# Optimization experiments

Hardware: AMD Instinct MI355X
Metric: run time of the kernel (lower is better)

Reference implementation:

```python
import jax, jax.numpy as jnp
import numpy as np
import math

D_MODEL = 512
N_TOTAL = 1024
HW = 4096
EPSILON = 0.2
NUM_HEADS = 8
D_K = D_MODEL // NUM_HEADS
BATCH = 4


def setup_inputs() -> dict:
    rng = jax.random.key(0)
    ks = jax.random.split(rng, 16)
    s = 1.0 / math.sqrt(D_MODEL)
    inp = {
        "query": jax.random.normal(ks[0], (BATCH, N_TOTAL, D_MODEL), jnp.float32),
        "key": jax.random.normal(ks[1], (BATCH, HW, D_MODEL), jnp.float32),
        "value": jax.random.normal(ks[2], (BATCH, HW, D_MODEL), jnp.float32),
        "x_tilde": jax.random.uniform(ks[3], (HW, 2), jnp.float32),
        "x_hat": jax.random.uniform(ks[4], (N_TOTAL, HW, 2), jnp.float32),
        # torch nn.Linear params: W is (out, in), y = x @ W.T + b
        "Wq": jax.random.uniform(ks[5], (D_MODEL, D_MODEL), jnp.float32, -s, s),
        "bq": jax.random.uniform(ks[6], (D_MODEL,), jnp.float32, -s, s),
        "Wk": jax.random.uniform(ks[7], (D_MODEL, D_MODEL), jnp.float32, -s, s),
        "bk": jax.random.uniform(ks[8], (D_MODEL,), jnp.float32, -s, s),
        "Wv": jax.random.uniform(ks[9], (D_MODEL, D_MODEL), jnp.float32, -s, s),
        "bv": jax.random.uniform(ks[10], (D_MODEL,), jnp.float32, -s, s),
        "Wo": jax.random.uniform(ks[11], (D_MODEL, D_MODEL), jnp.float32, -s, s),
        "bo": jax.random.uniform(ks[12], (D_MODEL,), jnp.float32, -s, s),
    }
    return inp


def _geo_mask(x_tilde, x_hat):
    # x_tilde: (HW, 2), x_hat: (N_total, HW, 2)
    diff = x_tilde[None, :, :] - x_hat            # (N, HW, 2)
    dist = jnp.sqrt(jnp.sum(diff * diff, axis=-1))  # (N, HW)
    return jnp.where(dist < EPSILON, 0.0, -jnp.inf).astype(x_hat.dtype)


def reference(query, key, value, x_tilde, x_hat, Wq, bq, Wk, bk, Wv, bv, Wo, bo):
    B = query.shape[0]
    M_geo = _geo_mask(x_tilde, x_hat)  # (N, HW)

    def heads(x, W, b):
        y = x @ W.T + b                                   # (B, L, D)
        return y.reshape(B, -1, NUM_HEADS, D_K).transpose(0, 2, 1, 3)  # (B, H, L, dk)

    Q = heads(query, Wq, bq)   # (B, H, N, dk)
    K = heads(key, Wk, bk)     # (B, H, HW, dk)
    V = heads(value, Wv, bv)   # (B, H, HW, dk)

    scores = jnp.einsum("bhnd,bhmd->bhnm", Q, K) / math.sqrt(D_K)
    scores = scores + M_geo[None, None, :, :]
    attn = jax.nn.softmax(scores, axis=-1)                # (B, H, N, HW)
    ctx = jnp.einsum("bhnm,bhmd->bhnd", attn, V)          # (B, H, N, dk)
    ctx = ctx.transpose(0, 2, 1, 3).reshape(B, -1, D_MODEL)
    out = ctx @ Wo.T + bo                                 # (B, N, D)
    return out, attn
```

## Files before the change

kernel.cpp:

```cpp
#include <hip/hip_runtime.h>
#include <cstdint>
#include <cstddef>

typedef __attribute__((ext_vector_type(4))) float f32x4;
typedef __attribute__((ext_vector_type(8))) short s16x8;
typedef __attribute__((ext_vector_type(4))) short s16x4;
typedef unsigned short u16;
typedef unsigned long long u64;

static __device__ inline u16 f2bf(float f) {
    unsigned u = __builtin_bit_cast(unsigned, f);
    u += 0x7fffu + ((u >> 16) & 1u);
    return (u16)(u >> 16);
}

static __device__ inline f32x4 mfma16(s16x8 a, s16x8 b, f32x4 c) {
    return __builtin_amdgcn_mfma_f32_16x16x32_bf16(a, b, c, 0, 0, 0);
}

static __device__ inline float redsum16(float v) {
    v += __shfl_xor(v, 1);
    v += __shfl_xor(v, 2);
    v += __shfl_xor(v, 4);
    v += __shfl_xor(v, 8);
    return v;
}

__global__ __launch_bounds__(256) void cvt_bf16_kernel(const float* __restrict__ src,
                                                       u16* __restrict__ dst, float scale) {
    int i = (blockIdx.x * 256 + threadIdx.x) * 4;
    f32x4 v = *(const f32x4*)(src + i);
    s16x4 o;
    o[0] = (short)f2bf(v[0] * scale); o[1] = (short)f2bf(v[1] * scale);
    o[2] = (short)f2bf(v[2] * scale); o[3] = (short)f2bf(v[3] * scale);
    *(s16x4*)(dst + i) = o;
}

__global__ __launch_bounds__(256) void mask_kernel(const float* __restrict__ xt,
                                                   const float* __restrict__ xh,
                                                   u64* __restrict__ mb) {
    int tid  = threadIdx.x;
    int lane = tid & 63;
    int wv   = blockIdx.x * 4 + (tid >> 6);
    int n    = wv >> 6;
    int mbk  = wv & 63;
    int m    = (mbk << 6) + lane;
    size_t hidx = ((size_t)n * 4096 + m) * 2;
    float dx = xt[2 * m]     - xh[hidx];
    float dy = xt[2 * m + 1] - xh[hidx + 1];
    bool p = sqrtf(dx * dx + dy * dy) < 0.2f;
    u64 bal = __ballot(p);
    if (lane == 0) mb[wv] = bal;
}

template <int INF32, int MODE, int LSHIFT>
__global__ __launch_bounds__(256) void proj_kernel(const void* __restrict__ Xv,
                                                   const u16* __restrict__ Wb,
                                                   const float* __restrict__ bias,
                                                   float bscale,
                                                   void* __restrict__ Yv) {
    __shared__ u16 aT[128 * 72];
    __shared__ u16 bT[128 * 72];

    int tid  = threadIdx.x;
    int lane = tid & 63, w = tid >> 6, q = lane >> 4, m15 = lane & 15;
    int wm = w >> 1, wn = w & 1;
    int m0 = blockIdx.x * 128, n0 = blockIdx.y * 128;
    int sRow = tid >> 1, sC = (tid & 1) * 32;

    f32x4 acc[4][4];
#pragma unroll
    for (int i = 0; i < 4; ++i)
#pragma unroll
        for (int j = 0; j < 4; ++j) { f32x4 z = {0.f, 0.f, 0.f, 0.f}; acc[i][j] = z; }

    for (int kb = 0; kb < 512; kb += 64) {
        if (INF32) {
            const float* X = (const float*)Xv;
#pragma unroll
            for (int j = 0; j < 8; ++j) {
                int col = sC + j * 4;
                f32x4 v = *(const f32x4*)(X + (size_t)(m0 + sRow) * 512 + kb + col);
                s16x4 o;
                o[0] = (short)f2bf(v[0]); o[1] = (short)f2bf(v[1]);
                o[2] = (short)f2bf(v[2]); o[3] = (short)f2bf(v[3]);
                *(s16x4*)(aT + sRow * 72 + col) = o;
            }
        } else {
            const u16* X = (const u16*)Xv;
#pragma unroll
            for (int j = 0; j < 4; ++j) {
                int col = sC + j * 8;
                s16x8 v = *(const s16x8*)(X + (size_t)(m0 + sRow) * 512 + kb + col);
                *(s16x8*)(aT + sRow * 72 + col) = v;
            }
        }
#pragma unroll
        for (int j = 0; j < 4; ++j) {
            int col = sC + j * 8;
            s16x8 v = *(const s16x8*)(Wb + (size_t)(n0 + sRow) * 512 + kb + col);
            *(s16x8*)(bT + sRow * 72 + col) = v;
        }
        __syncthreads();
#pragma unroll
        for (int kk = 0; kk < 2; ++kk) {
            s16x8 af[4], bf[4];
#pragma unroll
            for (int t = 0; t < 4; ++t) {
                af[t] = *(const s16x8*)(aT + (wm * 64 + t * 16 + m15) * 72 + kk * 32 + q * 8);
                bf[t] = *(const s16x8*)(bT + (wn * 64 + t * 16 + m15) * 72 + kk * 32 + q * 8);
            }
#pragma unroll
            for (int am = 0; am < 4; ++am)
#pragma unroll
                for (int bn = 0; bn < 4; ++bn)
                    acc[am][bn] = mfma16(af[am], bf[bn], acc[am][bn]);
        }
        __syncthreads();
    }

#pragma unroll
    for (int am = 0; am < 4; ++am) {
        int mg = m0 + wm * 64 + am * 16 + q * 4;
#pragma unroll
        for (int bn = 0; bn < 4; ++bn) {
            int col = n0 + wn * 64 + bn * 16 + m15;
            float bv = bias[col] * bscale;
            if (MODE == 2) {
                float* Y = (float*)Yv;
#pragma unroll
                for (int r = 0; r < 4; ++r)
                    Y[(size_t)(mg + r) * 512 + col] = acc[am][bn][r] + bv;
            } else if (MODE == 3) {
                u16* Y = (u16*)Yv;
                int hh = col >> 6, d = col & 63;
#pragma unroll
                for (int r = 0; r < 4; ++r) {
                    int m = mg + r;
                    int bb = m >> LSHIFT;
                    int nn = m & ((1 << LSHIFT) - 1);
                    Y[(((size_t)(bb * 8 + hh) << LSHIFT) + nn) * 64 + d] = f2bf(acc[am][bn][r] + bv);
                }
            } else {
                u16* Yt = (u16*)Yv;
                int bidx = mg >> 12, hw0 = mg & 4095;
                int hh = col >> 6, d = col & 63;
                s16x4 o;
#pragma unroll
                for (int r = 0; r < 4; ++r) o[r] = (short)f2bf(acc[am][bn][r] + bv);
                *(s16x4*)(Yt + ((size_t)((bidx << 3) + hh) * 64 + d) * 4096 + hw0) = o;
            }
        }
    }
}

__global__ __launch_bounds__(512) void attn_kernel(const u16* __restrict__ Qh,
                                                   const u16* __restrict__ Kh,
                                                   const u16* __restrict__ Vt,
                                                   const u64* __restrict__ mbits,
                                                   float* __restrict__ attnO,
                                                   u16* __restrict__ ctxO) {
    __shared__ u64   smask[2048];
    __shared__ float sred[8][32];
    __shared__ float srowi[32];
    __shared__ u16   sps[8][2][16 * 72];
    __shared__ float sctx[2048];

    int tid  = threadIdx.x;
    int lane = tid & 63, w = tid >> 6, q = lane >> 4, m15 = lane & 15;
    int i = blockIdx.x;
    int jj = i >> 3;
    int bh = (i & 7) * 4 + (jj & 3);
    int n0 = (jj >> 2) * 32;
    int b = bh >> 3, h = bh & 7;

    for (int t = tid; t < 2048; t += 512) {
        smask[t] = mbits[(size_t)n0 * 64 + t];
        sctx[t]  = 0.f;
    }
    __syncthreads();

    s16x8 aQ[2][2];
#pragma unroll
    for (int g = 0; g < 2; ++g) {
        const u16* Qp = Qh + (((size_t)bh << 10) + n0 + g * 16 + m15) * 64 + q * 8;
        aQ[g][0] = *(const s16x8*)(Qp);
        aQ[g][1] = *(const s16x8*)(Qp + 32);
    }

    const u16* Kp = Kh + (((size_t)bh << 12) + (w << 9) + m15) * 64 + q * 8;
    const float L2E = 1.44269504f;

    float ls[2][4] = {{0.f,0.f,0.f,0.f},{0.f,0.f,0.f,0.f}};
    for (int t4 = 0; t4 < 8; ++t4) {
        int widx = w * 8 + t4;
        u64 mk[2][4];
#pragma unroll
        for (int g = 0; g < 2; ++g)
#pragma unroll
            for (int r = 0; r < 4; ++r) mk[g][r] = smask[(g * 16 + q * 4 + r) * 64 + widx];
#pragma unroll
        for (int tt = 0; tt < 4; ++tt) {
            const u16* kp = Kp + (size_t)(t4 * 4 + tt) * (16 * 64);
            s16x8 b0 = *(const s16x8*)(kp);
            s16x8 b1 = *(const s16x8*)(kp + 32);
            f32x4 z = {0.f, 0.f, 0.f, 0.f};
            f32x4 c0 = mfma16(aQ[0][0], b0, mfma16(aQ[0][1], b1, z));
            f32x4 c1 = mfma16(aQ[1][0], b0, mfma16(aQ[1][1], b1, z));
            int bit = tt * 16 + m15;
#pragma unroll
            for (int r = 0; r < 4; ++r) {
                float p0 = ((mk[0][r] >> bit) & 1ull) ? exp2f(c0[r] * L2E) : 0.f;
                float p1 = ((mk[1][r] >> bit) & 1ull) ? exp2f(c1[r] * L2E) : 0.f;
                ls[0][r] += p0;
                ls[1][r] += p1;
            }
        }
    }
#pragma unroll
    for (int g = 0; g < 2; ++g)
#pragma unroll
        for (int r = 0; r < 4; ++r) {
            float v = redsum16(ls[g][r]);
            if (m15 == 0) sred[w][g * 16 + q * 4 + r] = v;
        }
    __syncthreads();
    if (tid < 32) {
        float ss = 0.f;
#pragma unroll
        for (int ww = 0; ww < 8; ++ww) ss += sred[ww][tid];
        srowi[tid] = 1.0f / ss;
    }
    __syncthreads();
    float iv[2][4];
#pragma unroll
    for (int g = 0; g < 2; ++g)
#pragma unroll
        for (int r = 0; r < 4; ++r) iv[g][r] = srowi[g * 16 + q * 4 + r];

    const u16* Vp = Vt + (((size_t)bh << 6) + m15) * 4096 + (w << 9) + q * 8;
    float* aBp[2];
#pragma unroll
    for (int g = 0; g < 2; ++g)
        aBp[g] = attnO + (((size_t)bh << 10) + n0 + g * 16 + q * 4) * 4096 + (w << 9) + m15;

    f32x4 ctxa[2][4];
#pragma unroll
    for (int g = 0; g < 2; ++g)
#pragma unroll
        for (int dt = 0; dt < 4; ++dt) { f32x4 z = {0.f, 0.f, 0.f, 0.f}; ctxa[g][dt] = z; }

    for (int cc = 0; cc < 8; ++cc) {
        int widx = w * 8 + cc;
        u64 mk[2][4];
#pragma unroll
        for (int g = 0; g < 2; ++g)
#pragma unroll
            for (int r = 0; r < 4; ++r) mk[g][r] = smask[(g * 16 + q * 4 + r) * 64 + widx];

        f32x4 cs[2][4];
#pragma unroll
        for (int tt = 0; tt < 4; ++tt) {
            const u16* kp = Kp + (size_t)(cc * 4 + tt) * (16 * 64);
            s16x8 b0 = *(const s16x8*)(kp);
            s16x8 b1 = *(const s16x8*)(kp + 32);
            f32x4 z = {0.f, 0.f, 0.f, 0.f};
            f32x4 c0 = mfma16(aQ[0][0], b0, mfma16(aQ[0][1], b1, z));
            f32x4 c1 = mfma16(aQ[1][0], b0, mfma16(aQ[1][1], b1, z));
            int bit = tt * 16 + m15;
#pragma unroll
            for (int r = 0; r < 4; ++r) {
                float p0 = ((mk[0][r] >> bit) & 1ull) ? exp2f(c0[r] * L2E) : 0.f;
                float p1 = ((mk[1][r] >> bit) & 1ull) ? exp2f(c1[r] * L2E) : 0.f;
                sps[w][0][(q * 4 + r) * 72 + tt * 16 + m15] = f2bf(p0);
                sps[w][1][(q * 4 + r) * 72 + tt * 16 + m15] = f2bf(p1);
                cs[0][tt][r] = p0 * iv[0][r];
                cs[1][tt][r] = p1 * iv[1][r];
            }
        }
#pragma unroll
        for (int g = 0; g < 2; ++g)
#pragma unroll
            for (int half = 0; half < 2; ++half) {
                s16x8 aP = *(const s16x8*)(&sps[w][g][m15 * 72 + half * 32 + q * 8]);
#pragma unroll
                for (int dt = 0; dt < 4; ++dt) {
                    s16x8 bV = *(const s16x8*)(Vp + (size_t)dt * (16 * 4096) + cc * 64 + half * 32);
                    ctxa[g][dt] = mfma16(aP, bV, ctxa[g][dt]);
                }
            }
#pragma unroll
        for (int g = 0; g < 2; ++g)
#pragma unroll
            for (int tt = 0; tt < 4; ++tt)
#pragma unroll
                for (int r = 0; r < 4; ++r)
                    aBp[g][(size_t)r * 4096 + cc * 64 + tt * 16] = cs[g][tt][r];
    }

#pragma unroll
    for (int g = 0; g < 2; ++g)
#pragma unroll
        for (int dt = 0; dt < 4; ++dt)
#pragma unroll
            for (int r = 0; r < 4; ++r)
                atomicAdd(&sctx[(g * 16 + q * 4 + r) * 64 + dt * 16 + m15],
                          ctxa[g][dt][r] * iv[g][r]);
    __syncthreads();
    for (int t = tid; t < 2048; t += 512) {
        int rr = t >> 6, d = t & 63;
        ctxO[(((size_t)b << 10) + n0 + rr) * 512 + h * 64 + d] = f2bf(sctx[t]);
    }
}

extern "C" void kernel_launch(void* const* d_in, const int* in_sizes, int n_in,
                              void* d_out, int out_size, void* d_ws, size_t ws_size,
                              hipStream_t stream) {
    (void)in_sizes; (void)n_in; (void)out_size; (void)ws_size;
    const float* query = (const float*)d_in[0];
    const float* key   = (const float*)d_in[1];
    const float* value = (const float*)d_in[2];
    const float* x_tilde = (const float*)d_in[3];
    const float* x_hat   = (const float*)d_in[4];
    const float* Wq = (const float*)d_in[5];  const float* bq = (const float*)d_in[6];
    const float* Wk = (const float*)d_in[7];  const float* bk = (const float*)d_in[8];
    const float* Wv = (const float*)d_in[9];  const float* bv = (const float*)d_in[10];
    const float* Wo = (const float*)d_in[11]; const float* bo = (const float*)d_in[12];

    char* ws = (char*)d_ws;
    u16* wq   = (u16*)(ws + 0);
    u16* wk   = (u16*)(ws + 524288);
    u16* wv   = (u16*)(ws + 1048576);
    u16* wo   = (u16*)(ws + 1572864);
    u16* Qh   = (u16*)(ws + 2097152);
    u16* Kh   = (u16*)(ws + 6291456);
    u16* Vtb  = (u16*)(ws + 23068672);
    u16* ctxb = (u16*)(ws + 39845888);
    u64* mbits = (u64*)(ws + 44040192);

    cvt_bf16_kernel<<<256, 256, 0, stream>>>(Wq, wq, 0.125f);
    cvt_bf16_kernel<<<256, 256, 0, stream>>>(Wk, wk, 1.0f);
    cvt_bf16_kernel<<<256, 256, 0, stream>>>(Wv, wv, 1.0f);
    cvt_bf16_kernel<<<256, 256, 0, stream>>>(Wo, wo, 1.0f);
    mask_kernel<<<16384, 256, 0, stream>>>(x_tilde, x_hat, mbits);

    proj_kernel<1, 3, 10><<<dim3(32, 4),  256, 0, stream>>>(query, wq, bq, 0.125f, Qh);
    proj_kernel<1, 3, 12><<<dim3(128, 4), 256, 0, stream>>>(key,   wk, bk, 1.0f,   Kh);
    proj_kernel<1, 1, 12><<<dim3(128, 4), 256, 0, stream>>>(value, wv, bv, 1.0f,   Vtb);

    float* attnO = (float*)d_out + 2097152;
    attn_kernel<<<1024, 512, 0, stream>>>(Qh, Kh, Vtb, mbits, attnO, ctxb);

    proj_kernel<0, 2, 10><<<dim3(32, 4), 256, 0, stream>>>(ctxb, wo, bo, 1.0f, d_out);
}
```

Before: 924.3 us.

## Cache unnormalized fp16 probabilities in registers instead of recomputing QK in attention

Attention now caches the packed fp16 exponentials from the first pass in registers, so the second pass no longer recomputes QK^T and exp. The whole pipeline moves from bf16 to fp16 MFMA. The block tile is halved to 16 query rows with twice as many blocks, and the large attention-matrix writes use nontemporal stores. In exchange there is higher register pressure (64 unsigneds per thread) and fp16 range limits on the exponentials, since scores are not max-subtracted and could overflow fp16.

```diff
diff --git a/kernel.cpp b/kernel.cpp
--- a/kernel.cpp
+++ b/kernel.cpp
@@ -3,19 +3,20 @@
 #include <cstddef>
 
 typedef __attribute__((ext_vector_type(4))) float f32x4;
+typedef __attribute__((ext_vector_type(8))) _Float16 h16x8;
+typedef __attribute__((ext_vector_type(2))) _Float16 h16x2;
 typedef __attribute__((ext_vector_type(8))) short s16x8;
 typedef __attribute__((ext_vector_type(4))) short s16x4;
 typedef unsigned short u16;
 typedef unsigned long long u64;
 
-static __device__ inline u16 f2bf(float f) {
-    unsigned u = __builtin_bit_cast(unsigned, f);
-    u += 0x7fffu + ((u >> 16) & 1u);
-    return (u16)(u >> 16);
-}
-
-static __device__ inline f32x4 mfma16(s16x8 a, s16x8 b, f32x4 c) {
-    return __builtin_amdgcn_mfma_f32_16x16x32_bf16(a, b, c, 0, 0, 0);
+static __device__ inline u16 f2h(float f) {
+    _Float16 h = (_Float16)f;
+    return __builtin_bit_cast(u16, h);
+}
+
+static __device__ inline f32x4 mfma16(h16x8 a, h16x8 b, f32x4 c) {
+    return __builtin_amdgcn_mfma_f32_16x16x32_f16(a, b, c, 0, 0, 0);
 }
 
 static __device__ inline float redsum16(float v) {
@@ -26,13 +27,13 @@
     return v;
 }
 
-__global__ __launch_bounds__(256) void cvt_bf16_kernel(const float* __restrict__ src,
-                                                       u16* __restrict__ dst, float scale) {
+__global__ __launch_bounds__(256) void cvt_h_kernel(const float* __restrict__ src,
+                                                    u16* __restrict__ dst, float scale) {
     int i = (blockIdx.x * 256 + threadIdx.x) * 4;
     f32x4 v = *(const f32x4*)(src + i);
     s16x4 o;
-    o[0] = (short)f2bf(v[0] * scale); o[1] = (short)f2bf(v[1] * scale);
-    o[2] = (short)f2bf(v[2] * scale); o[3] = (short)f2bf(v[3] * scale);
+    o[0] = (short)f2h(v[0] * scale); o[1] = (short)f2h(v[1] * scale);
+    o[2] = (short)f2h(v[2] * scale); o[3] = (short)f2h(v[3] * scale);
     *(s16x4*)(dst + i) = o;
 }
 
@@ -82,8 +83,8 @@
                 int col = sC + j * 4;
                 f32x4 v = *(const f32x4*)(X + (size_t)(m0 + sRow) * 512 + kb + col);
                 s16x4 o;
-                o[0] = (short)f2bf(v[0]); o[1] = (short)f2bf(v[1]);
-                o[2] = (short)f2bf(v[2]); o[3] = (short)f2bf(v[3]);
+                o[0] = (short)f2h(v[0]); o[1] = (short)f2h(v[1]);
+                o[2] = (short)f2h(v[2]); o[3] = (short)f2h(v[3]);
                 *(s16x4*)(aT + sRow * 72 + col) = o;
             }
         } else {
@@ -104,11 +105,11 @@
         __syncthreads();
 #pragma unroll
         for (int kk = 0; kk < 2; ++kk) {
-            s16x8 af[4], bf[4];
+            h16x8 af[4], bf[4];
 #pragma unroll
             for (int t = 0; t < 4; ++t) {
-                af[t] = *(const s16x8*)(aT + (wm * 64 + t * 16 + m15) * 72 + kk * 32 + q * 8);
-                bf[t] = *(const s16x8*)(bT + (wn * 64 + t * 16 + m15) * 72 + kk * 32 + q * 8);
+                af[t] = *(const h16x8*)(aT + (wm * 64 + t * 16 + m15) * 72 + kk * 32 + q * 8);
+                bf[t] = *(const h16x8*)(bT + (wn * 64 + t * 16 + m15) * 72 + kk * 32 + q * 8);
             }
 #pragma unroll
             for (int am = 0; am < 4; ++am)
@@ -139,7 +140,7 @@
                     int m = mg + r;
                     int bb = m >> LSHIFT;
                     int nn = m & ((1 << LSHIFT) - 1);
-                    Y[(((size_t)(bb * 8 + hh) << LSHIFT) + nn) * 64 + d] = f2bf(acc[am][bn][r] + bv);
+                    Y[(((size_t)(bb * 8 + hh) << LSHIFT) + nn) * 64 + d] = f2h(acc[am][bn][r] + bv);
                 }
             } else {
                 u16* Yt = (u16*)Yv;
@@ -147,7 +148,7 @@
                 int hh = col >> 6, d = col & 63;
                 s16x4 o;
 #pragma unroll
-                for (int r = 0; r < 4; ++r) o[r] = (short)f2bf(acc[am][bn][r] + bv);
+                for (int r = 0; r < 4; ++r) o[r] = (short)f2h(acc[am][bn][r] + bv);
                 *(s16x4*)(Yt + ((size_t)((bidx << 3) + hh) * 64 + d) * 4096 + hw0) = o;
             }
         }
@@ -160,156 +161,122 @@
                                                    const u64* __restrict__ mbits,
                                                    float* __restrict__ attnO,
                                                    u16* __restrict__ ctxO) {
-    __shared__ u64   smask[2048];
-    __shared__ float sred[8][32];
-    __shared__ float srowi[32];
-    __shared__ u16   sps[8][2][16 * 72];
-    __shared__ float sctx[2048];
+    __shared__ u64   smask[1024];
+    __shared__ float sred[8][16];
+    __shared__ float srowi[16];
+    __shared__ u16   sps[8][16 * 72];
+    __shared__ float sctx[1024];
 
     int tid  = threadIdx.x;
     int lane = tid & 63, w = tid >> 6, q = lane >> 4, m15 = lane & 15;
     int i = blockIdx.x;
     int jj = i >> 3;
     int bh = (i & 7) * 4 + (jj & 3);
-    int n0 = (jj >> 2) * 32;
+    int n0 = (jj >> 2) * 16;
     int b = bh >> 3, h = bh & 7;
 
-    for (int t = tid; t < 2048; t += 512) {
+    for (int t = tid; t < 1024; t += 512) {
         smask[t] = mbits[(size_t)n0 * 64 + t];
         sctx[t]  = 0.f;
     }
     __syncthreads();
 
-    s16x8 aQ[2][2];
-#pragma unroll
-    for (int g = 0; g < 2; ++g) {
-        const u16* Qp = Qh + (((size_t)bh << 10) + n0 + g * 16 + m15) * 64 + q * 8;
-        aQ[g][0] = *(const s16x8*)(Qp);
-        aQ[g][1] = *(const s16x8*)(Qp + 32);
+    h16x8 aQ[2];
+    {
+        const u16* Qp = Qh + (((size_t)bh << 10) + n0 + m15) * 64 + q * 8;
+        aQ[0] = *(const h16x8*)(Qp);
+        aQ[1] = *(const h16x8*)(Qp + 32);
     }
 
     const u16* Kp = Kh + (((size_t)bh << 12) + (w << 9) + m15) * 64 + q * 8;
     const float L2E = 1.44269504f;
 
-    float ls[2][4] = {{0.f,0.f,0.f,0.f},{0.f,0.f,0.f,0.f}};
-    for (int t4 = 0; t4 < 8; ++t4) {
-        int widx = w * 8 + t4;
-        u64 mk[2][4];
-#pragma unroll
-        for (int g = 0; g < 2; ++g)
-#pragma unroll
-            for (int r = 0; r < 4; ++r) mk[g][r] = smask[(g * 16 + q * 4 + r) * 64 + widx];
+    unsigned st[8][8];
+    float ls[4] = {0.f, 0.f, 0.f, 0.f};
+#pragma unroll
+    for (int cc = 0; cc < 8; ++cc) {
+        int widx = w * 8 + cc;
+        u64 mk[4];
+#pragma unroll
+        for (int r = 0; r < 4; ++r) mk[r] = smask[(q * 4 + r) * 64 + widx];
 #pragma unroll
         for (int tt = 0; tt < 4; ++tt) {
-            const u16* kp = Kp + (size_t)(t4 * 4 + tt) * (16 * 64);
-            s16x8 b0 = *(const s16x8*)(kp);
-            s16x8 b1 = *(const s16x8*)(kp + 32);
+            const u16* kp = Kp + (size_t)(cc * 4 + tt) * (16 * 64);
+            h16x8 b0 = *(const h16x8*)(kp);
+            h16x8 b1 = *(const h16x8*)(kp + 32);
             f32x4 z = {0.f, 0.f, 0.f, 0.f};
-            f32x4 c0 = mfma16(aQ[0][0], b0, mfma16(aQ[0][1], b1, z));
-            f32x4 c1 = mfma16(aQ[1][0], b0, mfma16(aQ[1][1], b1, z));
+            f32x4 c0 = mfma16(aQ[0], b0, mfma16(aQ[1], b1, z));
             int bit = tt * 16 + m15;
+            float p[4];
 #pragma unroll
             for (int r = 0; r < 4; ++r) {
-                float p0 = ((mk[0][r] >> bit) & 1ull) ? exp2f(c0[r] * L2E) : 0.f;
-                float p1 = ((mk[1][r] >> bit) & 1ull) ? exp2f(c1[r] * L2E) : 0.f;
-                ls[0][r] += p0;
-                ls[1][r] += p1;
-            }
-        }
-    }
-#pragma unroll
-    for (int g = 0; g < 2; ++g)
-#pragma unroll
-        for (int r = 0; r < 4; ++r) {
-            float v = redsum16(ls[g][r]);
-            if (m15 == 0) sred[w][g * 16 + q * 4 + r] = v;
-        }
+                p[r] = ((mk[r] >> bit) & 1ull) ? exp2f(c0[r] * L2E) : 0.f;
+                ls[r] += p[r];
+            }
+            st[cc][tt * 2 + 0] = __builtin_bit_cast(unsigned, __builtin_amdgcn_cvt_pkrtz(p[0], p[1]));
+            st[cc][tt * 2 + 1] = __builtin_bit_cast(unsigned, __builtin_amdgcn_cvt_pkrtz(p[2], p[3]));
+        }
+    }
+#pragma unroll
+    for (int r = 0; r < 4; ++r) {
+        float v = redsum16(ls[r]);
+        if (m15 == 0) sred[w][q * 4 + r] = v;
+    }
     __syncthreads();
-    if (tid < 32) {
+    if (tid < 16) {
         float ss = 0.f;
 #pragma unroll
         for (int ww = 0; ww < 8; ++ww) ss += sred[ww][tid];
         srowi[tid] = 1.0f / ss;
     }
     __syncthreads();
-    float iv[2][4];
-#pragma unroll
-    for (int g = 0; g < 2; ++g)
-#pragma unroll
-        for (int r = 0; r < 4; ++r) iv[g][r] = srowi[g * 16 + q * 4 + r];
+    float iv[4];
+#pragma unroll
+    for (int r = 0; r < 4; ++r) iv[r] = srowi[q * 4 + r];
 
     const u16* Vp = Vt + (((size_t)bh << 6) + m15) * 4096 + (w << 9) + q * 8;
-    float* aBp[2];
-#pragma unroll
-    for (int g = 0; g < 2; ++g)
-        aBp[g] = attnO + (((size_t)bh << 10) + n0 + g * 16 + q * 4) * 4096 + (w << 9) + m15;
-
-    f32x4 ctxa[2][4];
-#pragma unroll
-    for (int g = 0; g < 2; ++g)
-#pragma unroll
-        for (int dt = 0; dt < 4; ++dt) { f32x4 z = {0.f, 0.f, 0.f, 0.f}; ctxa[g][dt] = z; }
-
+    float* aBp = attnO + (((size_t)bh << 10) + n0 + q * 4) * 4096 + (w << 9) + m15;
+
+    f32x4 ctxa[4];
+#pragma unroll
+    for (int dt = 0; dt < 4; ++dt) { f32x4 z = {0.f, 0.f, 0.f, 0.f}; ctxa[dt] = z; }
+
+#pragma unroll
     for (int cc = 0; cc < 8; ++cc) {
-        int widx = w * 8 + cc;
-        u64 mk[2][4];
-#pragma unroll
-        for (int g = 0; g < 2; ++g)
-#pragma unroll
-            for (int r = 0; r < 4; ++r) mk[g][r] = smask[(g * 16 + q * 4 + r) * 64 + widx];
-
-        f32x4 cs[2][4];
 #pragma unroll
         for (int tt = 0; tt < 4; ++tt) {
-            const u16* kp = Kp + (size_t)(cc * 4 + tt) * (16 * 64);
-            s16x8 b0 = *(const s16x8*)(kp);
-            s16x8 b1 = *(const s16x8*)(kp + 32);
-            f32x4 z = {0.f, 0.f, 0.f, 0.f};
-            f32x4 c0 = mfma16(aQ[0][0], b0, mfma16(aQ[0][1], b1, z));
-            f32x4 c1 = mfma16(aQ[1][0], b0, mfma16(aQ[1][1], b1, z));
-            int bit = tt * 16 + m15;
-#pragma unroll
-            for (int r = 0; r < 4; ++r) {
-                float p0 = ((mk[0][r] >> bit) & 1ull) ? exp2f(c0[r] * L2E) : 0.f;
-                float p1 = ((mk[1][r] >> bit) & 1ull) ? exp2f(c1[r] * L2E) : 0.f;
-                sps[w][0][(q * 4 + r) * 72 + tt * 16 + m15] = f2bf(p0);
-                sps[w][1][(q * 4 + r) * 72 + tt * 16 + m15] = f2bf(p1);
-                cs[0][tt][r] = p0 * iv[0][r];
-                cs[1][tt][r] = p1 * iv[1][r];
-            }
-        }
-#pragma unroll
-        for (int g = 0; g < 2; ++g)
-#pragma unroll
-            for (int half = 0; half < 2; ++half) {
-                s16x8 aP = *(const s16x8*)(&sps[w][g][m15 * 72 + half * 32 + q * 8]);
-#pragma unroll
-                for (int dt = 0; dt < 4; ++dt) {
-                    s16x8 bV = *(const s16x8*)(Vp + (size_t)dt * (16 * 4096) + cc * 64 + half * 32);
-                    ctxa[g][dt] = mfma16(aP, bV, ctxa[g][dt]);
-                }
-            }
-#pragma unroll
-        for (int g = 0; g < 2; ++g)
-#pragma unroll
-            for (int tt = 0; tt < 4; ++tt)
-#pragma unroll
-                for (int r = 0; r < 4; ++r)
-                    aBp[g][(size_t)r * 4096 + cc * 64 + tt * 16] = cs[g][tt][r];
-    }
-
-#pragma unroll
-    for (int g = 0; g < 2; ++g)
-#pragma unroll
-        for (int dt = 0; dt < 4; ++dt)
-#pragma unroll
-            for (int r = 0; r < 4; ++r)
-                atomicAdd(&sctx[(g * 16 + q * 4 + r) * 64 + dt * 16 + m15],
-                          ctxa[g][dt][r] * iv[g][r]);
+#pragma unroll
+            for (int j = 0; j < 2; ++j) {
+                unsigned u = st[cc][tt * 2 + j];
+                sps[w][(q * 4 + j * 2 + 0) * 72 + tt * 16 + m15] = (u16)(u & 0xffffu);
+                sps[w][(q * 4 + j * 2 + 1) * 72 + tt * 16 + m15] = (u16)(u >> 16);
+                h16x2 hv = __builtin_bit_cast(h16x2, u);
+                float f0 = (float)hv[0] * iv[j * 2 + 0];
+                float f1 = (float)hv[1] * iv[j * 2 + 1];
+                __builtin_nontemporal_store(f0, aBp + (size_t)(j * 2 + 0) * 4096 + cc * 64 + tt * 16);
+                __builtin_nontemporal_store(f1, aBp + (size_t)(j * 2 + 1) * 4096 + cc * 64 + tt * 16);
+            }
+        }
+#pragma unroll
+        for (int half = 0; half < 2; ++half) {
+            h16x8 aP = *(const h16x8*)(&sps[w][m15 * 72 + half * 32 + q * 8]);
+#pragma unroll
+            for (int dt = 0; dt < 4; ++dt) {
+                h16x8 bV = *(const h16x8*)(Vp + (size_t)dt * (16 * 4096) + cc * 64 + half * 32);
+                ctxa[dt] = mfma16(aP, bV, ctxa[dt]);
+            }
+        }
+    }
+
+#pragma unroll
+    for (int dt = 0; dt < 4; ++dt)
+#pragma unroll
+        for (int r = 0; r < 4; ++r)
+            atomicAdd(&sctx[(q * 4 + r) * 64 + dt * 16 + m15], ctxa[dt][r] * iv[r]);
     __syncthreads();
-    for (int t = tid; t < 2048; t += 512) {
+    for (int t = tid; t < 1024; t += 512) {
         int rr = t >> 6, d = t & 63;
-        ctxO[(((size_t)b << 10) + n0 + rr) * 512 + h * 64 + d] = f2bf(sctx[t]);
+        ctxO[(((size_t)b << 10) + n0 + rr) * 512 + h * 64 + d] = f2h(sctx[t]);
     }
 }
 
@@ -338,10 +305,10 @@
     u16* ctxb = (u16*)(ws + 39845888);
     u64* mbits = (u64*)(ws + 44040192);
 
-    cvt_bf16_kernel<<<256, 256, 0, stream>>>(Wq, wq, 0.125f);
-    cvt_bf16_kernel<<<256, 256, 0, stream>>>(Wk, wk, 1.0f);
-    cvt_bf16_kernel<<<256, 256, 0, stream>>>(Wv, wv, 1.0f);
-    cvt_bf16_kernel<<<256, 256, 0, stream>>>(Wo, wo, 1.0f);
+    cvt_h_kernel<<<256, 256, 0, stream>>>(Wq, wq, 0.125f);
+    cvt_h_kernel<<<256, 256, 0, stream>>>(Wk, wk, 1.0f);
+    cvt_h_kernel<<<256, 256, 0, stream>>>(Wv, wv, 1.0f);
+    cvt_h_kernel<<<256, 256, 0, stream>>>(Wo, wo, 1.0f);
     mask_kernel<<<16384, 256, 0, stream>>>(x_tilde, x_hat, mbits);
 
     proj_kernel<1, 3, 10><<<dim3(32, 4),  256, 0, stream>>>(query, wq, bq, 0.125f, Qh);
@@ -349,7 +316,7 @@
     proj_kernel<1, 1, 12><<<dim3(128, 4), 256, 0, stream>>>(value, wv, bv, 1.0f,   Vtb);
 
     float* attnO = (float*)d_out + 2097152;
-    attn_kernel<<<1024, 512, 0, stream>>>(Qh, Kh, Vtb, mbits, attnO, ctxb);
+    attn_kernel<<<2048, 512, 0, stream>>>(Qh, Kh, Vtb, mbits, attnO, ctxb);
 
     proj_kernel<0, 2, 10><<<dim3(32, 4), 256, 0, stream>>>(ctxb, wo, bo, 1.0f, d_out);
 }
```

Result: slower. 985.9 us (+6.7%).

## Fuse attention passes into one QK pass, cache probabilities, switch to fp16 MFMA

Applied to the files above, without the earlier changes.

The attention kernel used to compute QK^T and exp twice: once for row sums and once for the normalized output and P·V. It now computes them once, accumulates P·V with unnormalized probabilities, and keeps packed fp16 probabilities in registers (st[8][4][2][2]). After the row sums are reduced it writes the normalized attn with nontemporal stores and scales ctx by the inverse sum. Every bf16 conversion and MFMA is switched to fp16, with launch_bounds(512,2) added. The cached probabilities add register pressure and may cause spills, and fp16 narrows the range available to exp values.

```diff
diff --git a/kernel.cpp b/kernel.cpp
--- a/kernel.cpp
+++ b/kernel.cpp
@@ -3,19 +3,20 @@
 #include <cstddef>
 
 typedef __attribute__((ext_vector_type(4))) float f32x4;
+typedef __attribute__((ext_vector_type(8))) _Float16 h16x8;
+typedef __attribute__((ext_vector_type(2))) _Float16 h16x2;
 typedef __attribute__((ext_vector_type(8))) short s16x8;
 typedef __attribute__((ext_vector_type(4))) short s16x4;
 typedef unsigned short u16;
 typedef unsigned long long u64;
 
-static __device__ inline u16 f2bf(float f) {
-    unsigned u = __builtin_bit_cast(unsigned, f);
-    u += 0x7fffu + ((u >> 16) & 1u);
-    return (u16)(u >> 16);
-}
-
-static __device__ inline f32x4 mfma16(s16x8 a, s16x8 b, f32x4 c) {
-    return __builtin_amdgcn_mfma_f32_16x16x32_bf16(a, b, c, 0, 0, 0);
+static __device__ inline u16 f2h(float f) {
+    _Float16 h = (_Float16)f;
+    return __builtin_bit_cast(u16, h);
+}
+
+static __device__ inline f32x4 mfma16(h16x8 a, h16x8 b, f32x4 c) {
+    return __builtin_amdgcn_mfma_f32_16x16x32_f16(a, b, c, 0, 0, 0);
 }
 
 static __device__ inline float redsum16(float v) {
@@ -26,13 +27,13 @@
     return v;
 }
 
-__global__ __launch_bounds__(256) void cvt_bf16_kernel(const float* __restrict__ src,
-                                                       u16* __restrict__ dst, float scale) {
+__global__ __launch_bounds__(256) void cvt_h_kernel(const float* __restrict__ src,
+                                                    u16* __restrict__ dst, float scale) {
     int i = (blockIdx.x * 256 + threadIdx.x) * 4;
     f32x4 v = *(const f32x4*)(src + i);
     s16x4 o;
-    o[0] = (short)f2bf(v[0] * scale); o[1] = (short)f2bf(v[1] * scale);
-    o[2] = (short)f2bf(v[2] * scale); o[3] = (short)f2bf(v[3] * scale);
+    o[0] = (short)f2h(v[0] * scale); o[1] = (short)f2h(v[1] * scale);
+    o[2] = (short)f2h(v[2] * scale); o[3] = (short)f2h(v[3] * scale);
     *(s16x4*)(dst + i) = o;
 }
 
@@ -82,8 +83,8 @@
                 int col = sC + j * 4;
                 f32x4 v = *(const f32x4*)(X + (size_t)(m0 + sRow) * 512 + kb + col);
                 s16x4 o;
-                o[0] = (short)f2bf(v[0]); o[1] = (short)f2bf(v[1]);
-                o[2] = (short)f2bf(v[2]); o[3] = (short)f2bf(v[3]);
+                o[0] = (short)f2h(v[0]); o[1] = (short)f2h(v[1]);
+                o[2] = (short)f2h(v[2]); o[3] = (short)f2h(v[3]);
                 *(s16x4*)(aT + sRow * 72 + col) = o;
             }
         } else {
@@ -104,11 +105,11 @@
         __syncthreads();
 #pragma unroll
         for (int kk = 0; kk < 2; ++kk) {
-            s16x8 af[4], bf[4];
+            h16x8 af[4], bf[4];
 #pragma unroll
             for (int t = 0; t < 4; ++t) {
-                af[t] = *(const s16x8*)(aT + (wm * 64 + t * 16 + m15) * 72 + kk * 32 + q * 8);
-                bf[t] = *(const s16x8*)(bT + (wn * 64 + t * 16 + m15) * 72 + kk * 32 + q * 8);
+                af[t] = *(const h16x8*)(aT + (wm * 64 + t * 16 + m15) * 72 + kk * 32 + q * 8);
+                bf[t] = *(const h16x8*)(bT + (wn * 64 + t * 16 + m15) * 72 + kk * 32 + q * 8);
             }
 #pragma unroll
             for (int am = 0; am < 4; ++am)
@@ -139,7 +140,7 @@
                     int m = mg + r;
                     int bb = m >> LSHIFT;
                     int nn = m & ((1 << LSHIFT) - 1);
-                    Y[(((size_t)(bb * 8 + hh) << LSHIFT) + nn) * 64 + d] = f2bf(acc[am][bn][r] + bv);
+                    Y[(((size_t)(bb * 8 + hh) << LSHIFT) + nn) * 64 + d] = f2h(acc[am][bn][r] + bv);
                 }
             } else {
                 u16* Yt = (u16*)Yv;
@@ -147,19 +148,19 @@
                 int hh = col >> 6, d = col & 63;
                 s16x4 o;
 #pragma unroll
-                for (int r = 0; r < 4; ++r) o[r] = (short)f2bf(acc[am][bn][r] + bv);
+                for (int r = 0; r < 4; ++r) o[r] = (short)f2h(acc[am][bn][r] + bv);
                 *(s16x4*)(Yt + ((size_t)((bidx << 3) + hh) * 64 + d) * 4096 + hw0) = o;
             }
         }
     }
 }
 
-__global__ __launch_bounds__(512) void attn_kernel(const u16* __restrict__ Qh,
-                                                   const u16* __restrict__ Kh,
-                                                   const u16* __restrict__ Vt,
-                                                   const u64* __restrict__ mbits,
-                                                   float* __restrict__ attnO,
-                                                   u16* __restrict__ ctxO) {
+__global__ __launch_bounds__(512, 2) void attn_kernel(const u16* __restrict__ Qh,
+                                                      const u16* __restrict__ Kh,
+                                                      const u16* __restrict__ Vt,
+                                                      const u64* __restrict__ mbits,
+                                                      float* __restrict__ attnO,
+                                                      u16* __restrict__ ctxO) {
     __shared__ u64   smask[2048];
     __shared__ float sred[8][32];
     __shared__ float srowi[32];
@@ -180,43 +181,78 @@
     }
     __syncthreads();
 
-    s16x8 aQ[2][2];
+    h16x8 aQ[2][2];
 #pragma unroll
     for (int g = 0; g < 2; ++g) {
         const u16* Qp = Qh + (((size_t)bh << 10) + n0 + g * 16 + m15) * 64 + q * 8;
-        aQ[g][0] = *(const s16x8*)(Qp);
-        aQ[g][1] = *(const s16x8*)(Qp + 32);
+        aQ[g][0] = *(const h16x8*)(Qp);
+        aQ[g][1] = *(const h16x8*)(Qp + 32);
     }
 
     const u16* Kp = Kh + (((size_t)bh << 12) + (w << 9) + m15) * 64 + q * 8;
+    const u16* Vp = Vt + (((size_t)bh << 6) + m15) * 4096 + (w << 9) + q * 8;
     const float L2E = 1.44269504f;
 
+    unsigned st[8][4][2][2];
     float ls[2][4] = {{0.f,0.f,0.f,0.f},{0.f,0.f,0.f,0.f}};
-    for (int t4 = 0; t4 < 8; ++t4) {
-        int widx = w * 8 + t4;
+    f32x4 ctxa[2][4];
+#pragma unroll
+    for (int g = 0; g < 2; ++g)
+#pragma unroll
+        for (int dt = 0; dt < 4; ++dt) { f32x4 z = {0.f, 0.f, 0.f, 0.f}; ctxa[g][dt] = z; }
+
+#pragma unroll
+    for (int cc = 0; cc < 8; ++cc) {
+        int widx = w * 8 + cc;
         u64 mk[2][4];
 #pragma unroll
         for (int g = 0; g < 2; ++g)
 #pragma unroll
             for (int r = 0; r < 4; ++r) mk[g][r] = smask[(g * 16 + q * 4 + r) * 64 + widx];
+
 #pragma unroll
         for (int tt = 0; tt < 4; ++tt) {
-            const u16* kp = Kp + (size_t)(t4 * 4 + tt) * (16 * 64);
-            s16x8 b0 = *(const s16x8*)(kp);
-            s16x8 b1 = *(const s16x8*)(kp + 32);
+            const u16* kp = Kp + (size_t)(cc * 4 + tt) * (16 * 64);
+            h16x8 b0 = *(const h16x8*)(kp);
+            h16x8 b1 = *(const h16x8*)(kp + 32);
             f32x4 z = {0.f, 0.f, 0.f, 0.f};
             f32x4 c0 = mfma16(aQ[0][0], b0, mfma16(aQ[0][1], b1, z));
             f32x4 c1 = mfma16(aQ[1][0], b0, mfma16(aQ[1][1], b1, z));
             int bit = tt * 16 + m15;
+            float p0[4], p1[4];
 #pragma unroll
             for (int r = 0; r < 4; ++r) {
-                float p0 = ((mk[0][r] >> bit) & 1ull) ? exp2f(c0[r] * L2E) : 0.f;
-                float p1 = ((mk[1][r] >> bit) & 1ull) ? exp2f(c1[r] * L2E) : 0.f;
-                ls[0][r] += p0;
-                ls[1][r] += p1;
-            }
-        }
-    }
+                p0[r] = ((mk[0][r] >> bit) & 1ull) ? exp2f(c0[r] * L2E) : 0.f;
+                p1[r] = ((mk[1][r] >> bit) & 1ull) ? exp2f(c1[r] * L2E) : 0.f;
+                ls[0][r] += p0[r];
+                ls[1][r] += p1[r];
+            }
+            st[cc][tt][0][0] = __builtin_bit_cast(unsigned, __builtin_amdgcn_cvt_pkrtz(p0[0], p0[1]));
+            st[cc][tt][0][1] = __builtin_bit_cast(unsigned, __builtin_amdgcn_cvt_pkrtz(p0[2], p0[3]));
+            st[cc][tt][1][0] = __builtin_bit_cast(unsigned, __builtin_amdgcn_cvt_pkrtz(p1[0], p1[1]));
+            st[cc][tt][1][1] = __builtin_bit_cast(unsigned, __builtin_amdgcn_cvt_pkrtz(p1[2], p1[3]));
+#pragma unroll
+            for (int g = 0; g < 2; ++g)
+#pragma unroll
+                for (int j = 0; j < 2; ++j) {
+                    unsigned u = st[cc][tt][g][j];
+                    sps[w][g][(q * 4 + 2 * j + 0) * 72 + tt * 16 + m15] = (u16)(u & 0xffffu);
+                    sps[w][g][(q * 4 + 2 * j + 1) * 72 + tt * 16 + m15] = (u16)(u >> 16);
+                }
+        }
+#pragma unroll
+        for (int g = 0; g < 2; ++g)
+#pragma unroll
+            for (int half = 0; half < 2; ++half) {
+                h16x8 aP = *(const h16x8*)(&sps[w][g][m15 * 72 + half * 32 + q * 8]);
+#pragma unroll
+                for (int dt = 0; dt < 4; ++dt) {
+                    h16x8 bV = *(const h16x8*)(Vp + (size_t)dt * (16 * 4096) + cc * 64 + half * 32);
+                    ctxa[g][dt] = mfma16(aP, bV, ctxa[g][dt]);
+                }
+            }
+    }
+
 #pragma unroll
     for (int g = 0; g < 2; ++g)
 #pragma unroll
@@ -238,64 +274,26 @@
 #pragma unroll
         for (int r = 0; r < 4; ++r) iv[g][r] = srowi[g * 16 + q * 4 + r];
 
-    const u16* Vp = Vt + (((size_t)bh << 6) + m15) * 4096 + (w << 9) + q * 8;
     float* aBp[2];
 #pragma unroll
     for (int g = 0; g < 2; ++g)
         aBp[g] = attnO + (((size_t)bh << 10) + n0 + g * 16 + q * 4) * 4096 + (w << 9) + m15;
 
-    f32x4 ctxa[2][4];
-#pragma unroll
-    for (int g = 0; g < 2; ++g)
-#pragma unroll
-        for (int dt = 0; dt < 4; ++dt) { f32x4 z = {0.f, 0.f, 0.f, 0.f}; ctxa[g][dt] = z; }
-
+#pragma unroll
     for (int cc = 0; cc < 8; ++cc) {
-        int widx = w * 8 + cc;
-        u64 mk[2][4];
-#pragma unroll
-        for (int g = 0; g < 2; ++g)
-#pragma unroll
-            for (int r = 0; r < 4; ++r) mk[g][r] = smask[(g * 16 + q * 4 + r) * 64 + widx];
-
-        f32x4 cs[2][4];
 #pragma unroll
         for (int tt = 0; tt < 4; ++tt) {
-            const u16* kp = Kp + (size_t)(cc * 4 + tt) * (16 * 64);
-            s16x8 b0 = *(const s16x8*)(kp);
-            s16x8 b1 = *(const s16x8*)(kp + 32);
-            f32x4 z = {0.f, 0.f, 0.f, 0.f};
-            f32x4 c0 = mfma16(aQ[0][0], b0, mfma16(aQ[0][1], b1, z));
-            f32x4 c1 = mfma16(aQ[1][0], b0, mfma16(aQ[1][1], b1, z));
-            int bit = tt * 16 + m15;
-#pragma unroll
-            for (int r = 0; r < 4; ++r) {
-                float p0 = ((mk[0][r] >> bit) & 1ull) ? exp2f(c0[r] * L2E) : 0.f;
-                float p1 = ((mk[1][r] >> bit) & 1ull) ? exp2f(c1[r] * L2E) : 0.f;
-                sps[w][0][(q * 4 + r) * 72 + tt * 16 + m15] = f2bf(p0);
-                sps[w][1][(q * 4 + r) * 72 + tt * 16 + m15] = f2bf(p1);
-                cs[0][tt][r] = p0 * iv[0][r];
-                cs[1][tt][r] = p1 * iv[1][r];
-            }
-        }
-#pragma unroll
-        for (int g = 0; g < 2; ++g)
-#pragma unroll
-            for (int half = 0; half < 2; ++half) {
-                s16x8 aP = *(const s16x8*)(&sps[w][g][m15 * 72 + half * 32 + q * 8]);
-#pragma unroll
-                for (int dt = 0; dt < 4; ++dt) {
-                    s16x8 bV = *(const s16x8*)(Vp + (size_t)dt * (16 * 4096) + cc * 64 + half * 32);
-                    ctxa[g][dt] = mfma16(aP, bV, ctxa[g][dt]);
+#pragma unroll
+            for (int g = 0; g < 2; ++g)
+#pragma unroll
+                for (int j = 0; j < 2; ++j) {
+                    h16x2 hv = __builtin_bit_cast(h16x2, st[cc][tt][g][j]);
+                    float f0 = (float)hv[0] * iv[g][2 * j + 0];
+                    float f1 = (float)hv[1] * iv[g][2 * j + 1];
+                    __builtin_nontemporal_store(f0, aBp[g] + (size_t)(2 * j + 0) * 4096 + cc * 64 + tt * 16);
+                    __builtin_nontemporal_store(f1, aBp[g] + (size_t)(2 * j + 1) * 4096 + cc * 64 + tt * 16);
                 }
-            }
-#pragma unroll
-        for (int g = 0; g < 2; ++g)
-#pragma unroll
-            for (int tt = 0; tt < 4; ++tt)
-#pragma unroll
-                for (int r = 0; r < 4; ++r)
-                    aBp[g][(size_t)r * 4096 + cc * 64 + tt * 16] = cs[g][tt][r];
+        }
     }
 
 #pragma unroll
@@ -309,7 +307,7 @@
     __syncthreads();
     for (int t = tid; t < 2048; t += 512) {
         int rr = t >> 6, d = t & 63;
-        ctxO[(((size_t)b << 10) + n0 + rr) * 512 + h * 64 + d] = f2bf(sctx[t]);
+        ctxO[(((size_t)b << 10) + n0 + rr) * 512 + h * 64 + d] = f2h(sctx[t]);
     }
 }
 
@@ -338,10 +336,10 @@
     u16* ctxb = (u16*)(ws + 39845888);
     u64* mbits = (u64*)(ws + 44040192);
 
-    cvt_bf16_kernel<<<256, 256, 0, stream>>>(Wq, wq, 0.125f);
-    cvt_bf16_kernel<<<256, 256, 0, stream>>>(Wk, wk, 1.0f);
-    cvt_bf16_kernel<<<256, 256, 0, stream>>>(Wv, wv, 1.0f);
-    cvt_bf16_kernel<<<256, 256, 0, stream>>>(Wo, wo, 1.0f);
+    cvt_h_kernel<<<256, 256, 0, stream>>>(Wq, wq, 0.125f);
+    cvt_h_kernel<<<256, 256, 0, stream>>>(Wk, wk, 1.0f);
+    cvt_h_kernel<<<256, 256, 0, stream>>>(Wv, wv, 1.0f);
+    cvt_h_kernel<<<256, 256, 0, stream>>>(Wo, wo, 1.0f);
     mask_kernel<<<16384, 256, 0, stream>>>(x_tilde, x_hat, mbits);
 
     proj_kernel<1, 3, 10><<<dim3(32, 4),  256, 0, stream>>>(query, wq, bq, 0.125f, Qh);
```

Result: slower. 1.103 ms (+19.3%).
